# Optimization experiments

Hardware: AMD Instinct MI355X
Metric: run time of the kernel (lower is better)

Reference implementation:

```python
import jax, jax.numpy as jnp
import numpy as np

N_NODES = 16500   # 100 battles x 165 hexes
N_EDGES = 100000  # per link type
K = 3             # number of link types (HeteroConv branches)
C_IN, C_HID, C_OUT = 170, 256, 256
GEN_EPS = 1e-7    # GENConv eps
BN_EPS = 1e-5     # BatchNorm1d eps


def setup_inputs() -> dict:
    key = jax.random.key(0)
    ki = iter(jax.random.split(key, 32))
    inp = {}
    inp["x"] = jax.random.normal(next(ki), (N_NODES, C_IN), jnp.float32)
    inp["edge_index"] = jax.random.randint(next(ki), (K, 2, N_EDGES), 0, N_NODES, dtype=jnp.int32)
    inp["edge_attr"] = jax.random.normal(next(ki), (K, N_EDGES, 1), jnp.float32)

    def uni(k, fan_in, shape):
        b = float(1.0 / np.sqrt(fan_in))
        return jax.random.uniform(k, shape, jnp.float32, -b, b)

    dims = [(C_IN, C_HID), (C_HID, C_HID), (C_HID, C_OUT)]
    for l, (ci, co) in enumerate(dims):
        inp[f"We{l}"] = uni(next(ki), 1, (K, 1, ci))          # edge encoder Linear(1, ci)
        inp[f"be{l}"] = jnp.zeros((K, ci), jnp.float32)
        inp[f"Wa{l}"] = uni(next(ki), ci, (K, ci, 2 * ci))     # MLP layer 1 (expansion=2)
        inp[f"ba{l}"] = jnp.zeros((K, 2 * ci), jnp.float32)
        inp[f"g{l}"] = jnp.ones((K, 2 * ci), jnp.float32)      # BatchNorm gamma
        inp[f"bt{l}"] = jnp.zeros((K, 2 * ci), jnp.float32)    # BatchNorm beta
        inp[f"Wb{l}"] = uni(next(ki), 2 * ci, (K, 2 * ci, co)) # MLP layer 2
        inp[f"bb{l}"] = jnp.zeros((K, co), jnp.float32)
    return inp


def _genconv(x, src, dst, ea, We, be, Wa, ba, g, bt, Wb, bb):
    """PyG GENConv (aggr='softmax', t=1, eps=1e-7, norm='batch') with self loops."""
    n = x.shape[0]
    loops = jnp.arange(n, dtype=src.dtype)
    src = jnp.concatenate([src, loops])
    dst = jnp.concatenate([dst, loops])
    ea = jnp.concatenate([ea, jnp.ones((n, ea.shape[1]), ea.dtype)], axis=0)
    e = ea @ We + be                           # [E+N, ci] edge encoder
    msg = jax.nn.relu(x[src] + e) + GEN_EPS    # [E+N, ci] message
    # per-destination, per-channel segment softmax aggregation
    mx = jax.ops.segment_max(msg, dst, num_segments=n)
    w = jnp.exp(msg - mx[dst])
    den = jax.ops.segment_sum(w, dst, num_segments=n)
    aggr = jax.ops.segment_sum(msg * w, dst, num_segments=n) / den
    out = aggr + x                             # residual with root node
    # MLP: Linear -> BatchNorm(train stats) -> ReLU -> Linear
    h = out @ Wa + ba
    mu = h.mean(axis=0)
    var = ((h - mu) ** 2).mean(axis=0)
    h = (h - mu) * jax.lax.rsqrt(var + BN_EPS) * g + bt
    h = jax.nn.relu(h)
    return h @ Wb + bb


_conv_k = jax.vmap(_genconv, in_axes=(None, 0, 0, 0, 0, 0, 0, 0, 0, 0, 0, 0))


def _forward(x, edge_index, edge_attr, layers):
    h = x
    for i, p in enumerate(layers):
        # HeteroConv: run GENConv per link type, sum-aggregate over types
        h = _conv_k(h, edge_index[:, 0], edge_index[:, 1], edge_attr, *p).sum(axis=0)
        if i < len(layers) - 1:
            h = jax.nn.leaky_relu(h, 0.01)
    return h


def reference(x, edge_index, edge_attr,
              We0, be0, Wa0, ba0, g0, bt0, Wb0, bb0,
              We1, be1, Wa1, ba1, g1, bt1, Wb1, bb1,
              We2, be2, Wa2, ba2, g2, bt2, Wb2, bb2):
    layers = [(We0, be0, Wa0, ba0, g0, bt0, Wb0, bb0),
              (We1, be1, Wa1, ba1, g1, bt1, Wb1, bb1),
              (We2, be2, Wa2, ba2, g2, bt2, Wb2, bb2)]
    return _forward(x, edge_index, edge_attr, layers)
```

## Files before the change

### kernel.cpp

```cpp
#include <hip/hip_runtime.h>
#include <math.h>

#define NN 16500
#define NP 16512
#define NE 100000
#define KT 3

typedef __attribute__((ext_vector_type(8))) short bf8_t;
typedef __attribute__((ext_vector_type(4))) float f4_t;

__device__ __forceinline__ unsigned short f2bf(float f) {
    unsigned int u = __float_as_uint(f);
    u += 0x7fffu + ((u >> 16) & 1u);
    return (unsigned short)(u >> 16);
}
__device__ __forceinline__ float bf2f(unsigned short h) {
    return __uint_as_float(((unsigned int)h) << 16);
}
__device__ __forceinline__ void gload16(unsigned short* lds, const unsigned short* g) {
    __builtin_amdgcn_global_load_lds(
        (const __attribute__((address_space(1))) void*)g,
        (__attribute__((address_space(3))) void*)lds, 16, 0, 0);
}


__global__ void deg_kernel(const int* __restrict__ ei, int* __restrict__ deg) {
    int t = blockIdx.x * blockDim.x + threadIdx.x;
    if (t >= KT * NE) return;
    int k = t / NE, e = t - k * NE;
    int d = ei[k * 2 * NE + NE + e];
    atomicAdd(&deg[k * NN + d], 1);
}

__global__ void scan_kernel(const int* __restrict__ deg, int* __restrict__ offs,
                            int* __restrict__ cursor) {
    int k = blockIdx.x;
    const int* dg = deg + k * NN;
    int* of = offs + k * (NN + 1);
    int* cu = cursor + k * NN;
    __shared__ int part[256];
    int tid = threadIdx.x;
    const int chunk = (NN + 255) / 256;
    int s0 = tid * chunk, s1 = min(NN, s0 + chunk);
    if (s0 > s1) s0 = s1;
    int sum = 0;
    for (int i = s0; i < s1; ++i) sum += dg[i];
    part[tid] = sum;
    __syncthreads();
    for (int off = 1; off < 256; off <<= 1) {
        int v = part[tid];
        int vp = (tid >= off) ? part[tid - off] : 0;
        __syncthreads();
        part[tid] = v + vp;
        __syncthreads();
    }
    int run = (tid == 0) ? 0 : part[tid - 1];
    for (int i = s0; i < s1; ++i) {
        of[i] = run; cu[i] = run;
        run += dg[i];
    }
    if (tid == 255) of[NN] = run;
}

__global__ void scatter_kernel(const int* __restrict__ ei, const float* __restrict__ ea,
                               int* __restrict__ cursor, int2* __restrict__ se) {
    int t = blockIdx.x * blockDim.x + threadIdx.x;
    if (t >= KT * NE) return;
    int k = t / NE, e = t - k * NE;
    int s = ei[k * 2 * NE + e];
    int d = ei[k * 2 * NE + NE + e];
    float a = ea[(size_t)k * NE + e];
    int pos = atomicAdd(&cursor[k * NN + d], 1);
    int2 p; p.x = s; p.y = __float_as_int(a);
    se[(size_t)k * NE + pos] = p;
}


template<int CI, bool BF16X>
__device__ __forceinline__ void loadrow4(float out[4], const void* xv, int s, int c0) {
    if (BF16X) {
        const unsigned short* xb = (const unsigned short*)xv;
        uint2 u = *(const uint2*)(xb + (size_t)s * CI + c0);
        out[0] = bf2f((unsigned short)(u.x & 0xffffu));
        out[1] = bf2f((unsigned short)(u.x >> 16));
        out[2] = bf2f((unsigned short)(u.y & 0xffffu));
        out[3] = bf2f((unsigned short)(u.y >> 16));
    } else {
        const float* p = (const float*)xv + (size_t)s * CI + c0;
        if (c0 + 4 <= CI) {
            float2 ab = *(const float2*)p;
            float2 cd = *(const float2*)(p + 2);
            out[0] = ab.x; out[1] = ab.y; out[2] = cd.x; out[3] = cd.y;
        } else {
            #pragma unroll
            for (int e = 0; e < 4; ++e) out[e] = (c0 + e < CI) ? p[e] : 0.f;
        }
    }
}

template<int CI, bool BF16X>
__global__ __launch_bounds__(256) void aggr_kernel(
    const void* __restrict__ xv, const int2* __restrict__ se_all,
    const int* __restrict__ offs_all,
    const float* __restrict__ We_all, const float* __restrict__ be_all,
    unsigned short* __restrict__ out_hi)
{
    constexpr int KP = (CI + 31) / 32 * 32;
    int k = blockIdx.y;
    int wv = threadIdx.x >> 6, lane = threadIdx.x & 63;
    int c0 = lane * 4;
    unsigned short* o = out_hi + (size_t)k * NP * KP;
    const int2*  se   = se_all + (size_t)k * NE;
    const int*   offs = offs_all + k * (NN + 1);
    const float* We   = We_all + (size_t)k * CI;
    const float* be   = be_all + (size_t)k * CI;

    constexpr bool ACT_ALL = (64 * 4 == KP) && (CI == KP);
    bool act = ACT_ALL || (c0 < CI);
    float w[4], b[4];
    #pragma unroll
    for (int e = 0; e < 4; ++e) {
        bool a = (c0 + e) < CI;
        w[e] = a ? We[c0 + e] : 0.f;
        b[e] = a ? be[c0 + e] : 0.f;
    }

    for (int it = 0; it < 4; ++it) {
        int d = blockIdx.x * 16 + it * 4 + wv;
        if (d >= NN) {
            if (c0 < KP) { uint2 z = {0u, 0u}; *(uint2*)(o + (size_t)d * KP + c0) = z; }
            continue;
        }
        float xd[4] = {0.f, 0.f, 0.f, 0.f};
        if (act) loadrow4<CI, BF16X>(xd, xv, d, c0);
        #pragma unroll
        for (int e = 0; e < 4; ++e) if ((c0 + e) >= CI) xd[e] = 0.f;

        float den[4], num[4];
        #pragma unroll
        for (int e = 0; e < 4; ++e) {
            float mg = fmaxf(xd[e] + w[e] + b[e], 0.f);
            float ex = __expf(mg);
            den[e] = ex;
            num[e] = mg * ex;
        }

        auto step = [&](const float xc[4], float a) {
            #pragma unroll
            for (int e = 0; e < 4; ++e) {
                float t = xc[e] + fmaf(a, w[e], b[e]);
                float mg = fmaxf(t, 0.f);
                float ex = __expf(mg);
                den[e] += ex;
                num[e] = fmaf(mg, ex, num[e]);
            }
        };

        int start = offs[d], end = offs[d + 1];
        for (int base = start; base < end; base += 64) {
            int cnt = min(64, end - base);
            int sv = 0; float av = 0.f;
            if (lane < cnt) {
                int2 p = se[base + lane];
                sv = p.x; av = __int_as_float(p.y);
            }
            float x0[4] = {0.f,0.f,0.f,0.f}, x1[4] = {0.f,0.f,0.f,0.f};
            float x2[4] = {0.f,0.f,0.f,0.f}, x3[4] = {0.f,0.f,0.f,0.f};
            {
                int sA = __shfl(sv, 0), sB = __shfl(sv, 1);
                int sC = __shfl(sv, 2), sD = __shfl(sv, 3);
                if (act)            loadrow4<CI, BF16X>(x0, xv, sA, c0);
                if (act && cnt > 1) loadrow4<CI, BF16X>(x1, xv, sB, c0);
                if (act && cnt > 2) loadrow4<CI, BF16X>(x2, xv, sC, c0);
                if (act && cnt > 3) loadrow4<CI, BF16X>(x3, xv, sD, c0);
            }
            int j = 0;
            for (; j + 3 < cnt; j += 4) {
                float a0 = __shfl(av, j),     a1 = __shfl(av, j + 1);
                float a2 = __shfl(av, j + 2), a3 = __shfl(av, j + 3);
                int s4 = __shfl(sv, (j + 4) & 63), s5 = __shfl(sv, (j + 5) & 63);
                int s6 = __shfl(sv, (j + 6) & 63), s7 = __shfl(sv, (j + 7) & 63);
                step(x0, a0);
                if (act && (j + 4) < cnt) loadrow4<CI, BF16X>(x0, xv, s4, c0);
                step(x1, a1);
                if (act && (j + 5) < cnt) loadrow4<CI, BF16X>(x1, xv, s5, c0);
                step(x2, a2);
                if (act && (j + 6) < cnt) loadrow4<CI, BF16X>(x2, xv, s6, c0);
                step(x3, a3);
                if (act && (j + 7) < cnt) loadrow4<CI, BF16X>(x3, xv, s7, c0);
            }
            if (j < cnt)     step(x0, __shfl(av, j));
            if (j + 1 < cnt) step(x1, __shfl(av, j + 1));
            if (j + 2 < cnt) step(x2, __shfl(av, j + 2));
        }
        if (c0 < KP) {
            unsigned short r[4];
            #pragma unroll
            for (int e = 0; e < 4; ++e) {
                float v = ((c0 + e) < CI) ? (num[e] / den[e] + xd[e]) : 0.f;
                r[e] = f2bf(v);
            }
            uint2 pk = {(unsigned)r[0] | ((unsigned)r[1] << 16),
                        (unsigned)r[2] | ((unsigned)r[3] << 16)};
            *(uint2*)(o + (size_t)d * KP + c0) = pk;
        }
    }
}


struct SplitJob { const float* W; unsigned short* out; int kdim, ndim, np_, kp; };
struct SplitJobs { SplitJob j[6]; };

__global__ void split_all_kernel(SplitJobs jobs) {
    SplitJob jb = jobs.j[blockIdx.z];
    int idx = blockIdx.x * 256 + threadIdx.x;
    int total = KT * jb.np_ * jb.kp;
    if (idx >= total) return;
    int k = idx / (jb.np_ * jb.kp);
    int rem = idx - k * jb.np_ * jb.kp;
    int n = rem / jb.kp;
    int kk = rem - n * jb.kp;
    float v = (n < jb.ndim && kk < jb.kdim) ? jb.W[((size_t)k * jb.kdim + kk) * jb.ndim + n] : 0.f;
    jb.out[idx] = f2bf(v);
}


__global__ __launch_bounds__(256, 3) void gemm1_mfma(
    const unsigned short* __restrict__ A_hi,
    const unsigned short* __restrict__ B_hi,
    const float* __restrict__ bias_all, unsigned short* __restrict__ C_all,
    float* __restrict__ psum,
    int KP, int ldc, int Mv, int Nv)
{
    __shared__ unsigned short Ah[2][128 * 32];
    __shared__ unsigned short Bh[2][128 * 32];

    int z = blockIdx.z;
    int gxT = gridDim.x, gyT = gridDim.y;
    int NHP = gxT * 128;
    const unsigned short* Ahg = A_hi + (size_t)z * NP * KP;
    const unsigned short* Bhg = B_hi + (size_t)z * NHP * KP;
    const float* bias = bias_all + (size_t)z * Nv;
    unsigned short* C = C_all + (size_t)z * NP * ldc;

    int tid = threadIdx.x;
    int w = tid >> 6, l = tid & 63;
    int bm = blockIdx.y * 128, bn = blockIdx.x * 128;
    int lane15 = l & 15, quad = l >> 4;
    int wm = (w >> 1) * 64, wn = (w & 1) * 64;
    int srow = l & 15;
    int scol = (l >> 4) * 8;

    f4_t acc[4][4];
    #pragma unroll
    for (int i = 0; i < 4; ++i)
        #pragma unroll
        for (int j = 0; j < 4; ++j) { f4_t zz = {0.f,0.f,0.f,0.f}; acc[i][j] = zz; }

    size_t aoff0 = (size_t)(bm + 32 * w +  0 + srow) * KP + scol;
    size_t aoff1 = (size_t)(bm + 32 * w + 16 + srow) * KP + scol;
    size_t boff0 = (size_t)(bn + 32 * w +  0 + srow) * KP + scol;
    size_t boff1 = (size_t)(bn + 32 * w + 16 + srow) * KP + scol;
    int rb0 = 32 * w, rb1 = 32 * w + 16;
    int ta = (w >> 1) * 4, tb = (w & 1) * 4;

    gload16(&Ah[0][rb0 * 32], Ahg + aoff0);
    gload16(&Ah[0][rb1 * 32], Ahg + aoff1);
    gload16(&Bh[0][rb0 * 32], Bhg + boff0);
    gload16(&Bh[0][rb1 * 32], Bhg + boff1);
    __syncthreads();

    int cur = 0;
    for (int k0 = 32; k0 < KP; k0 += 32) {
        int nxt = cur ^ 1;
        gload16(&Ah[nxt][rb0 * 32], Ahg + aoff0 + k0);
        gload16(&Ah[nxt][rb1 * 32], Ahg + aoff1 + k0);
        gload16(&Bh[nxt][rb0 * 32], Bhg + boff0 + k0);
        gload16(&Bh[nxt][rb1 * 32], Bhg + boff1 + k0);

        bf8_t fa[4], fb[4];
        #pragma unroll
        for (int i = 0; i < 4; ++i) {
            fa[i] = *(const bf8_t*)&Ah[cur][(ta + i) * 512 + l * 8];
            fb[i] = *(const bf8_t*)&Bh[cur][(tb + i) * 512 + l * 8];
        }
        #pragma unroll
        for (int i = 0; i < 4; ++i)
            #pragma unroll
            for (int j = 0; j < 4; ++j)
                acc[i][j] = __builtin_amdgcn_mfma_f32_16x16x32_bf16(fa[i], fb[j], acc[i][j], 0, 0, 0);
        __syncthreads();
        cur = nxt;
    }
    {
        bf8_t fa[4], fb[4];
        #pragma unroll
        for (int i = 0; i < 4; ++i) {
            fa[i] = *(const bf8_t*)&Ah[cur][(ta + i) * 512 + l * 8];
            fb[i] = *(const bf8_t*)&Bh[cur][(tb + i) * 512 + l * 8];
        }
        #pragma unroll
        for (int i = 0; i < 4; ++i)
            #pragma unroll
            for (int j = 0; j < 4; ++j)
                acc[i][j] = __builtin_amdgcn_mfma_f32_16x16x32_bf16(fa[i], fb[j], acc[i][j], 0, 0, 0);
    }

    #pragma unroll
    for (int j = 0; j < 4; ++j) {
        int c = bn + wn + j * 16 + lane15;
        float bc = (c < Nv) ? bias[c] : 0.f;
        float s1 = 0.f, s2 = 0.f;
        #pragma unroll
        for (int i = 0; i < 4; ++i) {
            #pragma unroll
            for (int r5 = 0; r5 < 4; ++r5) {
                int r = bm + wm + i * 16 + quad * 4 + r5;
                float v = acc[i][j][r5] + bc;
                unsigned short q = f2bf(v);
                if (r < Mv && c < Nv) C[(size_t)r * ldc + c] = q;
                bool ok = (r < NN) && (c < Nv);
                float vq = ok ? bf2f(q) : 0.f;
                s1 += vq;
                s2 = fmaf(vq, vq, s2);
            }
        }
        s1 += __shfl_xor(s1, 16); s2 += __shfl_xor(s2, 16);
        s1 += __shfl_xor(s1, 32); s2 += __shfl_xor(s2, 32);
        if (quad == 0) {
            int wrow = w >> 1;
            int col = wn + j * 16 + lane15;
            size_t o = ((((size_t)z * gyT + blockIdx.y) * gxT + blockIdx.x) * 2 + wrow) * 256 + col * 2;
            float2 st = {s1, s2};
            *(float2*)&psum[o] = st;
        }
    }
}


__global__ __launch_bounds__(256) void finalize_kernel(
    const float* __restrict__ psum,
    const float* __restrict__ g_all, const float* __restrict__ bt_all,
    float* __restrict__ scale_all, float* __restrict__ shift_all,
    int hid, int gxT)
{
    int z = blockIdx.x;
    int t64 = threadIdx.x & 63;
    int slice = threadIdx.x >> 6;
    int c = blockIdx.y * 64 + t64;
    __shared__ double rs1[4][64];
    __shared__ double rs2[4][64];
    double s1 = 0.0, s2 = 0.0;
    if (c < gxT * 128) {
        int gx = c >> 7, col = c & 127;
        for (int gy = slice; gy < NP / 128; gy += 4) {
            size_t base = (((size_t)z * (NP / 128) + gy) * gxT + gx) * 2 * 256 + col * 2;
            float2 a  = *(const float2*)&psum[base];
            float2 b2 = *(const float2*)&psum[base + 256];
            s1 += (double)a.x + b2.x;
            s2 += (double)a.y + b2.y;
        }
    }
    rs1[slice][t64] = s1;
    rs2[slice][t64] = s2;
    __syncthreads();
    if (slice == 0 && c < hid) {
        double S1 = rs1[0][t64] + rs1[1][t64] + rs1[2][t64] + rs1[3][t64];
        double S2 = rs2[0][t64] + rs2[1][t64] + rs2[2][t64] + rs2[3][t64];
        double mu = S1 / NN;
        double var = S2 / NN - mu * mu;
        if (var < 0.0) var = 0.0;
        float rs = (float)(1.0 / sqrt(var + 1e-5));
        float sc = rs * g_all[(size_t)z * hid + c];
        scale_all[(size_t)z * 512 + c] = sc;
        shift_all[(size_t)z * 512 + c] = bt_all[(size_t)z * hid + c] - (float)mu * sc;
    }
}


__device__ __forceinline__ bf8_t bnpack(uint4 hv, float4 s0, float4 s1,
                                        float4 t0, float4 t1, int ch0, int hid) {
    unsigned int uu[4] = {hv.x, hv.y, hv.z, hv.w};
    float ss[8] = {s0.x, s0.y, s0.z, s0.w, s1.x, s1.y, s1.z, s1.w};
    float tt[8] = {t0.x, t0.y, t0.z, t0.w, t1.x, t1.y, t1.z, t1.w};
    bf8_t r;
    #pragma unroll
    for (int e = 0; e < 8; ++e) {
        unsigned short hb = (e & 1) ? (unsigned short)(uu[e >> 1] >> 16)
                                    : (unsigned short)(uu[e >> 1] & 0xffffu);
        float x = bf2f(hb);
        float val = (ch0 + e < hid) ? fmaxf(fmaf(x, ss[e], tt[e]), 0.f) : 0.f;
        r[e] = (short)f2bf(val);
    }
    return r;
}

__global__ __launch_bounds__(256, 4) void gemm2_mfma(
    const unsigned short* __restrict__ h_all, const float* __restrict__ scale_all,
    const float* __restrict__ shift_all,
    const unsigned short* __restrict__ B_hi,
    const float* __restrict__ bb,
    float* __restrict__ outf, unsigned short* __restrict__ outb,
    int KP, int hid, int leaky, int as_bf16)
{
    __shared__ unsigned short Ah[2][2048];
    __shared__ unsigned short Bh[2][8192];

    int tid = threadIdx.x;
    int w = tid >> 6, l = tid & 63;
    int bm = blockIdx.y * 32, bn = blockIdx.x * 128;
    int lane15 = l & 15, quad = l >> 4;
    int srow = l & 15, scol = (l >> 4) * 8;

    const int KPZ = KP / 64;
    const int NIT = 3 * KPZ;

    f4_t acc[2][2];
    #pragma unroll
    for (int i = 0; i < 2; ++i)
        #pragma unroll
        for (int j = 0; j < 2; ++j) { f4_t zz = {0.f,0.f,0.f,0.f}; acc[i][j] = zz; }

    int asub = tid >> 7;
    int arb  = (tid >> 6) & 1;
    int grow = arb * 16 + (tid & 15);
    int ccol = asub * 32 + ((tid >> 4) & 3) * 8;
    size_t arow = (size_t)(bm + grow) * KP;
    int adst = tid * 8;

    size_t brow[4]; int bdst[4];
    #pragma unroll
    for (int s2 = 0; s2 < 2; ++s2)
        #pragma unroll
        for (int g = 0; g < 2; ++g) {
            brow[s2 * 2 + g] = (size_t)(bn + 32 * w + g * 16 + srow) * KP + s2 * 32 + scol;
            bdst[s2 * 2 + g] = s2 * 4096 + (2 * w + g) * 512;
        }

    {
        uint4 hv = *(const uint4*)(h_all + arow + ccol);
        #pragma unroll
        for (int q = 0; q < 4; ++q)
            gload16(&Bh[0][bdst[q]], B_hi + brow[q]);
        float4 s0 = *(const float4*)(scale_all + ccol);
        float4 s1 = *(const float4*)(scale_all + ccol + 4);
        float4 t0 = *(const float4*)(shift_all + ccol);
        float4 t1 = *(const float4*)(shift_all + ccol + 4);
        *(bf8_t*)&Ah[0][adst] = bnpack(hv, s0, s1, t0, t1, ccol, hid);
    }
    __syncthreads();

    int cur = 0;
    for (int it = 0; it < NIT; ++it) {
        int nit = it + 1;
        bool have = nit < NIT;
        int nxt = cur ^ 1;
        uint4 hv;
        float4 s0, s1, t0, t1;
        int nch = 0;
        if (have) {
            int nz = nit / KPZ, nkk = (nit - nz * KPZ) * 64;
            nch = nkk + ccol;
            hv = *(const uint4*)(h_all + (size_t)nz * NP * KP + arow + nch);
            const float* scl = scale_all + (size_t)nz * 512 + nch;
            const float* shf = shift_all + (size_t)nz * 512 + nch;
            s0 = *(const float4*)scl; s1 = *(const float4*)(scl + 4);
            t0 = *(const float4*)shf; t1 = *(const float4*)(shf + 4);
            const unsigned short* bz = B_hi + (size_t)nz * 256 * KP + nkk;
            #pragma unroll
            for (int q = 0; q < 4; ++q)
                gload16(&Bh[nxt][bdst[q]], bz + brow[q]);
        }
        #pragma unroll
        for (int s2 = 0; s2 < 2; ++s2) {
            bf8_t fa[2], fb[2];
            fa[0] = *(const bf8_t*)&Ah[cur][s2 * 1024 + 0 * 512 + l * 8];
            fa[1] = *(const bf8_t*)&Ah[cur][s2 * 1024 + 1 * 512 + l * 8];
            fb[0] = *(const bf8_t*)&Bh[cur][s2 * 4096 + (2 * w + 0) * 512 + l * 8];
            fb[1] = *(const bf8_t*)&Bh[cur][s2 * 4096 + (2 * w + 1) * 512 + l * 8];
            #pragma unroll
            for (int i = 0; i < 2; ++i)
                #pragma unroll
                for (int j = 0; j < 2; ++j)
                    acc[i][j] = __builtin_amdgcn_mfma_f32_16x16x32_bf16(fa[i], fb[j], acc[i][j], 0, 0, 0);
        }
        if (have)
            *(bf8_t*)&Ah[nxt][adst] = bnpack(hv, s0, s1, t0, t1, nch, hid);
        __syncthreads();
        cur = nxt;
    }

    #pragma unroll
    for (int j = 0; j < 2; ++j) {
        int c = bn + w * 32 + j * 16 + lane15;
        float bsum = bb[c] + bb[256 + c] + bb[512 + c];
        #pragma unroll
        for (int i = 0; i < 2; ++i) {
            #pragma unroll
            for (int r5 = 0; r5 < 4; ++r5) {
                int r = bm + i * 16 + quad * 4 + r5;
                if (r < NN) {
                    float v = acc[i][j][r5] + bsum;
                    if (leaky) v = (v > 0.f) ? v : 0.01f * v;
                    if (as_bf16) outb[(size_t)r * 256 + c] = f2bf(v);
                    else         outf[(size_t)r * 256 + c] = v;
                }
            }
        }
    }
}


extern "C" void kernel_launch(void* const* d_in, const int* in_sizes, int n_in,
                              void* d_out, int out_size, void* d_ws, size_t ws_size,
                              hipStream_t stream)
{
    const float* x  = (const float*)d_in[0];
    const int*   ei = (const int*)d_in[1];
    const float* ea = (const float*)d_in[2];

    char* w = (char*)d_ws;
    auto alloc = [&](size_t bytes) {
        char* p = w;
        w += (bytes + 255) & ~(size_t)255;
        return p;
    };
    int* deg    = (int*)alloc((size_t)KT * NN * 4);
    int* offs   = (int*)alloc((size_t)KT * (NN + 1) * 4);
    int* cursor = (int*)alloc((size_t)KT * NN * 4);
    int2* se    = (int2*)alloc((size_t)KT * NE * 8);
    unsigned short* a1_hi = (unsigned short*)alloc((size_t)KT * NP * 256 * 2);
    unsigned short* h3 = (unsigned short*)alloc((size_t)KT * NP * 512 * 2);
    unsigned short* bta_l[3];
    unsigned short* btb_l[3];
    for (int l = 0; l < 3; ++l) {
        bta_l[l] = (unsigned short*)alloc((size_t)KT * 512 * 256 * 2);
        btb_l[l] = (unsigned short*)alloc((size_t)KT * 256 * 512 * 2);
    }
    float* psum = (float*)alloc((size_t)KT * (NP / 128) * 4 * 2 * 256 * 4);
    float* scale3 = (float*)alloc((size_t)KT * 512 * 4);
    float* shift3 = (float*)alloc((size_t)KT * 512 * 4);
    unsigned short* bufA = (unsigned short*)alloc((size_t)NN * 256 * 2);
    unsigned short* bufB = (unsigned short*)alloc((size_t)NN * 256 * 2);

    hipMemsetAsync(deg, 0, (size_t)KT * NN * 4, stream);
    int net = KT * NE;
    deg_kernel<<<(net + 255) / 256, 256, 0, stream>>>(ei, deg);
    scan_kernel<<<KT, 256, 0, stream>>>(deg, offs, cursor);
    scatter_kernel<<<(net + 255) / 256, 256, 0, stream>>>(ei, ea, cursor, se);

    SplitJobs jobs;
    int maxtot = 0;
    for (int l = 0; l < 3; ++l) {
        int ci  = (l == 0) ? 170 : 256;
        int KP1 = (ci + 31) / 32 * 32;
        int hid = 2 * ci;
        int NHP = (hid + 127) / 128 * 128;
        int KP2 = (hid + 63) / 64 * 64;
        jobs.j[2 * l]     = { (const float*)d_in[3 + 8 * l + 2], bta_l[l], ci,  hid, NHP, KP1 };
        jobs.j[2 * l + 1] = { (const float*)d_in[3 + 8 * l + 6], btb_l[l], hid, 256, 256, KP2 };
        maxtot = max(maxtot, KT * NHP * KP1);
        maxtot = max(maxtot, KT * 256 * KP2);
    }
    dim3 gsp((maxtot + 255) / 256, 1, 6);
    split_all_kernel<<<gsp, 256, 0, stream>>>(jobs);

    const void* hin = x;
    for (int l = 0; l < 3; ++l) {
        int ci  = (l == 0) ? 170 : 256;
        int KP1 = (ci + 31) / 32 * 32;
        int hid = 2 * ci;
        int NHP = (hid + 127) / 128 * 128;
        int KP2 = (hid + 63) / 64 * 64;
        const float* We = (const float*)d_in[3 + 8 * l + 0];
        const float* be = (const float*)d_in[3 + 8 * l + 1];
        const float* ba = (const float*)d_in[3 + 8 * l + 3];
        const float* g  = (const float*)d_in[3 + 8 * l + 4];
        const float* bt = (const float*)d_in[3 + 8 * l + 5];
        const float* bb = (const float*)d_in[3 + 8 * l + 7];

        dim3 ga(NP / 16, KT);
        if (l == 0)
            aggr_kernel<170, false><<<ga, 256, 0, stream>>>(hin, se, offs, We, be, a1_hi);
        else
            aggr_kernel<256, true><<<ga, 256, 0, stream>>>(hin, se, offs, We, be, a1_hi);

        dim3 g1(NHP / 128, NP / 128, KT);
        gemm1_mfma<<<g1, 256, 0, stream>>>(a1_hi, bta_l[l], ba, h3, psum, KP1, KP2, NN, hid);

        dim3 gf(KT, 8);
        finalize_kernel<<<gf, 256, 0, stream>>>(psum, g, bt, scale3, shift3, hid, NHP / 128);

        unsigned short* outb = (l == 0) ? bufA : bufB;
        dim3 g2(2, NP / 32);
        gemm2_mfma<<<g2, 256, 0, stream>>>(h3, scale3, shift3, btb_l[l], bb,
                                           (float*)d_out, outb, KP2, hid,
                                           (l < 2) ? 1 : 0, (l < 2) ? 1 : 0);

        hin = (l < 2) ? (const void*)outb : nullptr;
    }
}
```

Baseline: 749.7 us.

## Recompute first GEMM in fused BN-ReLU-GEMM2 kernel instead of storing hidden activations

The first GEMM now only computes BatchNorm column statistics and no longer writes the bf16 hidden tensor. A new fused kernel recomputes Linear1 per 64-row tile, applies bias, BN scale/shift and ReLU, stages the result in LDS, and feeds it directly into the second GEMM, summing over the three link types. This removes the large hidden-tensor write and re-read at the cost of doing the first GEMM twice, reading Wa/Wb fragments straight from global memory, and running fewer blocks with lower occupancy. BN statistics now come from fp32 values rather than bf16-rounded ones.

```diff
diff --git a/kernel.cpp b/kernel.cpp
--- a/kernel.cpp
+++ b/kernel.cpp
@@ -225,12 +225,12 @@
 }
 
 
-__global__ __launch_bounds__(256, 3) void gemm1_mfma(
+__global__ __launch_bounds__(256, 3) void gemm1_stats(
     const unsigned short* __restrict__ A_hi,
     const unsigned short* __restrict__ B_hi,
-    const float* __restrict__ bias_all, unsigned short* __restrict__ C_all,
+    const float* __restrict__ bias_all,
     float* __restrict__ psum,
-    int KP, int ldc, int Mv, int Nv)
+    int KP, int Nv)
 {
     __shared__ unsigned short Ah[2][128 * 32];
     __shared__ unsigned short Bh[2][128 * 32];
@@ -241,7 +241,6 @@
     const unsigned short* Ahg = A_hi + (size_t)z * NP * KP;
     const unsigned short* Bhg = B_hi + (size_t)z * NHP * KP;
     const float* bias = bias_all + (size_t)z * Nv;
-    unsigned short* C = C_all + (size_t)z * NP * ldc;
 
     int tid = threadIdx.x;
     int w = tid >> 6, l = tid & 63;
@@ -316,13 +315,10 @@
             #pragma unroll
             for (int r5 = 0; r5 < 4; ++r5) {
                 int r = bm + wm + i * 16 + quad * 4 + r5;
-                float v = acc[i][j][r5] + bc;
-                unsigned short q = f2bf(v);
-                if (r < Mv && c < Nv) C[(size_t)r * ldc + c] = q;
                 bool ok = (r < NN) && (c < Nv);
-                float vq = ok ? bf2f(q) : 0.f;
-                s1 += vq;
-                s2 = fmaf(vq, vq, s2);
+                float v = ok ? (acc[i][j][r5] + bc) : 0.f;
+                s1 += v;
+                s2 = fmaf(v, v, s2);
             }
         }
         s1 += __shfl_xor(s1, 16); s2 += __shfl_xor(s2, 16);
@@ -378,135 +374,119 @@
 }
 
 
-__device__ __forceinline__ bf8_t bnpack(uint4 hv, float4 s0, float4 s1,
-                                        float4 t0, float4 t1, int ch0, int hid) {
-    unsigned int uu[4] = {hv.x, hv.y, hv.z, hv.w};
-    float ss[8] = {s0.x, s0.y, s0.z, s0.w, s1.x, s1.y, s1.z, s1.w};
-    float tt[8] = {t0.x, t0.y, t0.z, t0.w, t1.x, t1.y, t1.z, t1.w};
-    bf8_t r;
-    #pragma unroll
-    for (int e = 0; e < 8; ++e) {
-        unsigned short hb = (e & 1) ? (unsigned short)(uu[e >> 1] >> 16)
-                                    : (unsigned short)(uu[e >> 1] & 0xffffu);
-        float x = bf2f(hb);
-        float val = (ch0 + e < hid) ? fmaxf(fmaf(x, ss[e], tt[e]), 0.f) : 0.f;
-        r[e] = (short)f2bf(val);
-    }
-    return r;
-}
-
-__global__ __launch_bounds__(256, 4) void gemm2_mfma(
-    const unsigned short* __restrict__ h_all, const float* __restrict__ scale_all,
+template<int KP1, int HP>
+__global__ __launch_bounds__(256, 2) void fused_mid(
+    const unsigned short* __restrict__ a1,
+    const unsigned short* __restrict__ Wat,
+    const unsigned short* __restrict__ Wbt,
+    const float* __restrict__ ba_all,
+    const float* __restrict__ scale_all,
     const float* __restrict__ shift_all,
-    const unsigned short* __restrict__ B_hi,
     const float* __restrict__ bb,
     float* __restrict__ outf, unsigned short* __restrict__ outb,
-    int KP, int hid, int leaky, int as_bf16)
+    int hid, int leaky, int as_bf16)
 {
-    __shared__ unsigned short Ah[2][2048];
-    __shared__ unsigned short Bh[2][8192];
-
-    int tid = threadIdx.x;
-    int w = tid >> 6, l = tid & 63;
-    int bm = blockIdx.y * 32, bn = blockIdx.x * 128;
+    constexpr int NKS = KP1 / 32;
+    constexpr int NSL = HP / 128;
+    __shared__ unsigned short Ah[NKS * 4 * 512];
+    __shared__ unsigned short Hb[2][64 * 130];
+
+    int tid = threadIdx.x, w = tid >> 6, l = tid & 63;
     int lane15 = l & 15, quad = l >> 4;
-    int srow = l & 15, scol = (l >> 4) * 8;
-
-    const int KPZ = KP / 64;
-    const int NIT = 3 * KPZ;
-
-    f4_t acc[2][2];
+    int bm = blockIdx.x * 64;
+
+    f4_t outacc[4][4];
     #pragma unroll
-    for (int i = 0; i < 2; ++i)
-        #pragma unroll
-        for (int j = 0; j < 2; ++j) { f4_t zz = {0.f,0.f,0.f,0.f}; acc[i][j] = zz; }
-
-    int asub = tid >> 7;
-    int arb  = (tid >> 6) & 1;
-    int grow = arb * 16 + (tid & 15);
-    int ccol = asub * 32 + ((tid >> 4) & 3) * 8;
-    size_t arow = (size_t)(bm + grow) * KP;
-    int adst = tid * 8;
-
-    size_t brow[4]; int bdst[4];
+    for (int i = 0; i < 4; ++i)
+        #pragma unroll
+        for (int j = 0; j < 4; ++j) { f4_t zz = {0.f,0.f,0.f,0.f}; outacc[i][j] = zz; }
+
+    for (int z = 0; z < KT; ++z) {
+        const unsigned short* Az  = a1  + (size_t)z * NP * KP1;
+        const unsigned short* Waz = Wat + (size_t)z * HP * KP1;
+        const unsigned short* Wbz = Wbt + (size_t)z * 256 * HP;
+        const float* scl = scale_all + z * 512;
+        const float* shf = shift_all + z * 512;
+        const float* baz = ba_all + (size_t)z * hid;
+
+        #pragma unroll
+        for (int ks = 0; ks < NKS; ++ks)
+            gload16(&Ah[(ks * 4 + w) * 512 + l * 8],
+                    Az + (size_t)(bm + 16 * w + lane15) * KP1 + ks * 32 + quad * 8);
+        __syncthreads();
+
+        #pragma unroll
+        for (int s = 0; s < NSL; ++s) {
+            int c2w = s * 128 + w * 32;
+            f4_t hacc[4][2];
+            #pragma unroll
+            for (int i = 0; i < 4; ++i)
+                #pragma unroll
+                for (int j = 0; j < 2; ++j) { f4_t zz = {0.f,0.f,0.f,0.f}; hacc[i][j] = zz; }
+            #pragma unroll
+            for (int ks = 0; ks < NKS; ++ks) {
+                bf8_t wa0 = *(const bf8_t*)(Waz + (size_t)(c2w + lane15) * KP1 + ks * 32 + quad * 8);
+                bf8_t wa1 = *(const bf8_t*)(Waz + (size_t)(c2w + 16 + lane15) * KP1 + ks * 32 + quad * 8);
+                #pragma unroll
+                for (int rb = 0; rb < 4; ++rb) {
+                    bf8_t af = *(const bf8_t*)&Ah[(ks * 4 + rb) * 512 + l * 8];
+                    hacc[rb][0] = __builtin_amdgcn_mfma_f32_16x16x32_bf16(af, wa0, hacc[rb][0], 0, 0, 0);
+                    hacc[rb][1] = __builtin_amdgcn_mfma_f32_16x16x32_bf16(af, wa1, hacc[rb][1], 0, 0, 0);
+                }
+            }
+            unsigned short* hb = &Hb[s & 1][0];
+            #pragma unroll
+            for (int jn = 0; jn < 2; ++jn) {
+                int c2 = c2w + jn * 16 + lane15;
+                bool okc = c2 < hid;
+                float bax = okc ? baz[c2] : 0.f;
+                float sc  = okc ? scl[c2] : 0.f;
+                float sh  = okc ? shf[c2] : 0.f;
+                int colw = w * 32 + jn * 16 + lane15;
+                #pragma unroll
+                for (int rb = 0; rb < 4; ++rb)
+                    #pragma unroll
+                    for (int r5 = 0; r5 < 4; ++r5) {
+                        float v = fmaxf(fmaf(hacc[rb][jn][r5] + bax, sc, sh), 0.f);
+                        int row = rb * 16 + quad * 4 + r5;
+                        hb[row * 130 + colw] = f2bf(v);
+                    }
+            }
+            __syncthreads();
+            #pragma unroll
+            for (int t = 0; t < 4; ++t) {
+                bf8_t hf[4];
+                #pragma unroll
+                for (int rb = 0; rb < 4; ++rb)
+                    hf[rb] = *(const bf8_t*)&hb[(rb * 16 + lane15) * 130 + t * 32 + quad * 8];
+                #pragma unroll
+                for (int jc = 0; jc < 4; ++jc) {
+                    bf8_t wb = *(const bf8_t*)(Wbz + (size_t)(64 * w + jc * 16 + lane15) * HP
+                                               + s * 128 + t * 32 + quad * 8);
+                    #pragma unroll
+                    for (int rb = 0; rb < 4; ++rb)
+                        outacc[rb][jc] = __builtin_amdgcn_mfma_f32_16x16x32_bf16(hf[rb], wb, outacc[rb][jc], 0, 0, 0);
+                }
+            }
+        }
+    }
+
     #pragma unroll
-    for (int s2 = 0; s2 < 2; ++s2)
-        #pragma unroll
-        for (int g = 0; g < 2; ++g) {
-            brow[s2 * 2 + g] = (size_t)(bn + 32 * w + g * 16 + srow) * KP + s2 * 32 + scol;
-            bdst[s2 * 2 + g] = s2 * 4096 + (2 * w + g) * 512;
-        }
-
-    {
-        uint4 hv = *(const uint4*)(h_all + arow + ccol);
-        #pragma unroll
-        for (int q = 0; q < 4; ++q)
-            gload16(&Bh[0][bdst[q]], B_hi + brow[q]);
-        float4 s0 = *(const float4*)(scale_all + ccol);
-        float4 s1 = *(const float4*)(scale_all + ccol + 4);
-        float4 t0 = *(const float4*)(shift_all + ccol);
-        float4 t1 = *(const float4*)(shift_all + ccol + 4);
-        *(bf8_t*)&Ah[0][adst] = bnpack(hv, s0, s1, t0, t1, ccol, hid);
-    }
-    __syncthreads();
-
-    int cur = 0;
-    for (int it = 0; it < NIT; ++it) {
-        int nit = it + 1;
-        bool have = nit < NIT;
-        int nxt = cur ^ 1;
-        uint4 hv;
-        float4 s0, s1, t0, t1;
-        int nch = 0;
-        if (have) {
-            int nz = nit / KPZ, nkk = (nit - nz * KPZ) * 64;
-            nch = nkk + ccol;
-            hv = *(const uint4*)(h_all + (size_t)nz * NP * KP + arow + nch);
-            const float* scl = scale_all + (size_t)nz * 512 + nch;
-            const float* shf = shift_all + (size_t)nz * 512 + nch;
-            s0 = *(const float4*)scl; s1 = *(const float4*)(scl + 4);
-            t0 = *(const float4*)shf; t1 = *(const float4*)(shf + 4);
-            const unsigned short* bz = B_hi + (size_t)nz * 256 * KP + nkk;
-            #pragma unroll
-            for (int q = 0; q < 4; ++q)
-                gload16(&Bh[nxt][bdst[q]], bz + brow[q]);
-        }
-        #pragma unroll
-        for (int s2 = 0; s2 < 2; ++s2) {
-            bf8_t fa[2], fb[2];
-            fa[0] = *(const bf8_t*)&Ah[cur][s2 * 1024 + 0 * 512 + l * 8];
-            fa[1] = *(const bf8_t*)&Ah[cur][s2 * 1024 + 1 * 512 + l * 8];
-            fb[0] = *(const bf8_t*)&Bh[cur][s2 * 4096 + (2 * w + 0) * 512 + l * 8];
-            fb[1] = *(const bf8_t*)&Bh[cur][s2 * 4096 + (2 * w + 1) * 512 + l * 8];
-            #pragma unroll
-            for (int i = 0; i < 2; ++i)
-                #pragma unroll
-                for (int j = 0; j < 2; ++j)
-                    acc[i][j] = __builtin_amdgcn_mfma_f32_16x16x32_bf16(fa[i], fb[j], acc[i][j], 0, 0, 0);
-        }
-        if (have)
-            *(bf8_t*)&Ah[nxt][adst] = bnpack(hv, s0, s1, t0, t1, nch, hid);
-        __syncthreads();
-        cur = nxt;
-    }
-
-    #pragma unroll
-    for (int j = 0; j < 2; ++j) {
-        int c = bn + w * 32 + j * 16 + lane15;
+    for (int jc = 0; jc < 4; ++jc) {
+        int c = 64 * w + jc * 16 + lane15;
         float bsum = bb[c] + bb[256 + c] + bb[512 + c];
         #pragma unroll
-        for (int i = 0; i < 2; ++i) {
+        for (int rb = 0; rb < 4; ++rb)
             #pragma unroll
             for (int r5 = 0; r5 < 4; ++r5) {
-                int r = bm + i * 16 + quad * 4 + r5;
+                int r = bm + rb * 16 + quad * 4 + r5;
                 if (r < NN) {
-                    float v = acc[i][j][r5] + bsum;
+                    float v = outacc[rb][jc][r5] + bsum;
                     if (leaky) v = (v > 0.f) ? v : 0.01f * v;
                     if (as_bf16) outb[(size_t)r * 256 + c] = f2bf(v);
                     else         outf[(size_t)r * 256 + c] = v;
                 }
             }
-        }
     }
 }
 
@@ -530,7 +510,6 @@
     int* cursor = (int*)alloc((size_t)KT * NN * 4);
     int2* se    = (int2*)alloc((size_t)KT * NE * 8);
     unsigned short* a1_hi = (unsigned short*)alloc((size_t)KT * NP * 256 * 2);
-    unsigned short* h3 = (unsigned short*)alloc((size_t)KT * NP * 512 * 2);
     unsigned short* bta_l[3];
     unsigned short* btb_l[3];
     for (int l = 0; l < 3; ++l) {
@@ -556,7 +535,7 @@
         int KP1 = (ci + 31) / 32 * 32;
         int hid = 2 * ci;
         int NHP = (hid + 127) / 128 * 128;
-        int KP2 = (hid + 63) / 64 * 64;
+        int KP2 = NHP;
         jobs.j[2 * l]     = { (const float*)d_in[3 + 8 * l + 2], bta_l[l], ci,  hid, NHP, KP1 };
         jobs.j[2 * l + 1] = { (const float*)d_in[3 + 8 * l + 6], btb_l[l], hid, 256, 256, KP2 };
         maxtot = max(maxtot, KT * NHP * KP1);
@@ -571,7 +550,6 @@
         int KP1 = (ci + 31) / 32 * 32;
         int hid = 2 * ci;
         int NHP = (hid + 127) / 128 * 128;
-        int KP2 = (hid + 63) / 64 * 64;
         const float* We = (const float*)d_in[3 + 8 * l + 0];
         const float* be = (const float*)d_in[3 + 8 * l + 1];
         const float* ba = (const float*)d_in[3 + 8 * l + 3];
@@ -586,16 +564,20 @@
             aggr_kernel<256, true><<<ga, 256, 0, stream>>>(hin, se, offs, We, be, a1_hi);
 
         dim3 g1(NHP / 128, NP / 128, KT);
-        gemm1_mfma<<<g1, 256, 0, stream>>>(a1_hi, bta_l[l], ba, h3, psum, KP1, KP2, NN, hid);
+        gemm1_stats<<<g1, 256, 0, stream>>>(a1_hi, bta_l[l], ba, psum, KP1, hid);
 
         dim3 gf(KT, 8);
         finalize_kernel<<<gf, 256, 0, stream>>>(psum, g, bt, scale3, shift3, hid, NHP / 128);
 
         unsigned short* outb = (l == 0) ? bufA : bufB;
-        dim3 g2(2, NP / 32);
-        gemm2_mfma<<<g2, 256, 0, stream>>>(h3, scale3, shift3, btb_l[l], bb,
-                                           (float*)d_out, outb, KP2, hid,
-                                           (l < 2) ? 1 : 0, (l < 2) ? 1 : 0);
+        if (l == 0)
+            fused_mid<192, 384><<<NP / 64, 256, 0, stream>>>(
+                a1_hi, bta_l[l], btb_l[l], ba, scale3, shift3, bb,
+                (float*)d_out, outb, hid, 1, 1);
+        else
+            fused_mid<256, 512><<<NP / 64, 256, 0, stream>>>(
+                a1_hi, bta_l[l], btb_l[l], ba, scale3, shift3, bb,
+                (float*)d_out, outb, hid, (l < 2) ? 1 : 0, (l < 2) ? 1 : 0);
 
         hin = (l < 2) ? (const void*)outb : nullptr;
     }
```

Measured after the change: 747.6 us. About the same (-0.3%).
